# Performance work log

Hardware: AMD Instinct MI355X
Metric: run time of the kernel (lower is better)

Reference implementation:

```python
import jax, jax.numpy as jnp
import numpy as np

N_EMBD = 512
NUM_HEADS = 8
HEAD_SIZE = 64


def setup_inputs() -> dict:
    key = jax.random.key(0)
    ks = jax.random.split(key, 6)
    B, T, C, H, D = 64, 256, N_EMBD, NUM_HEADS, HEAD_SIZE
    s = 0.02
    return {
        "x": jax.random.normal(ks[0], (B, T, C), dtype=jnp.float32),
        "wq": jax.random.normal(ks[1], (H, C, D), dtype=jnp.float32) * s,
        "wk": jax.random.normal(ks[2], (H, C, D), dtype=jnp.float32) * s,
        "wv": jax.random.normal(ks[3], (H, C, D), dtype=jnp.float32) * s,
        "bq": jnp.zeros((H, D), dtype=jnp.float32),
        "bk": jnp.zeros((H, D), dtype=jnp.float32),
        "bv": jnp.zeros((H, D), dtype=jnp.float32),
        "wo": jax.random.normal(ks[4], (H * D, C), dtype=jnp.float32) * s,
        "bo": jnp.zeros((C,), dtype=jnp.float32),
    }


def reference(x, wq, wk, wv, bq, bk, bv, wo, bo):
    B, T, C = x.shape
    H, _, D = wq.shape
    # per-head QKV projections (vectorized over heads)
    q = jnp.einsum('btc,hcd->bhtd', x, wq) + bq[None, :, None, :]
    k = jnp.einsum('btc,hcd->bhtd', x, wk) + bk[None, :, None, :]
    v = jnp.einsum('btc,hcd->bhtd', x, wv) + bv[None, :, None, :]
    scale = 1.0 / jnp.sqrt(jnp.asarray(D, dtype=x.dtype))
    scores = jnp.einsum('bhtd,bhsd->bhts', q, k) * scale  # [B,H,T,T]
    causal = jnp.tril(jnp.ones((T, T), dtype=bool))
    scores = jnp.where(causal[None, None], scores, -jnp.inf)
    weights = jax.nn.softmax(scores, axis=-1)  # dropout omitted (eval mode)
    out = jnp.einsum('bhts,bhsd->bhtd', weights, v)  # [B,H,T,D]
    combined = out.transpose(0, 2, 1, 3).reshape(B, T, H * D)
    return combined @ wo + bo
```

## Files before the change

### kernel.cpp

```cpp
#include <hip/hip_runtime.h>

typedef unsigned int   u32;
typedef unsigned short u16;
typedef __attribute__((ext_vector_type(8))) short short8;
typedef __attribute__((ext_vector_type(4))) float f32x4;


__device__ __forceinline__ u16 f2bf(float f) {
    u32 u = __float_as_uint(f);
    u += 0x7fffu + ((u >> 16) & 1u);
    return (u16)(u >> 16);
}

__device__ __forceinline__ void gload_lds16(const u16* g, u16* l) {
    __builtin_amdgcn_global_load_lds(
        (const __attribute__((address_space(1))) u32*)(const void*)g,
        (__attribute__((address_space(3))) u32*)(void*)l, 16, 0, 0);
}

__global__ void cast_x_kernel(const float* __restrict__ x, u16* __restrict__ xb) {
    int i = blockIdx.x * 256 + threadIdx.x;
    float4 v = ((const float4*)x)[i];
    ushort4 o;
    o.x = f2bf(v.x); o.y = f2bf(v.y); o.z = f2bf(v.z); o.w = f2bf(v.w);
    ((ushort4*)xb)[i] = o;
}

__global__ void pack_wqkv_kernel(const float* __restrict__ wq, const float* __restrict__ wk,
                                 const float* __restrict__ wv, u16* __restrict__ wt) {
    int i = blockIdx.x * 256 + threadIdx.x;
    int n = i >> 9, c = i & 511;
    int proj = n >> 9, hd = n & 511;
    int h = hd >> 6, d = hd & 63;
    const float* w = (proj == 0) ? wq : (proj == 1) ? wk : wv;
    wt[(size_t)n * 512 + c] = f2bf(w[h * 32768 + c * 64 + d]);
}

__global__ void pack_wo_kernel(const float* __restrict__ wo, u16* __restrict__ wt) {
    int i = blockIdx.x * 256 + threadIdx.x;
    int n = i >> 9, k = i & 511;
    wt[(size_t)n * 512 + k] = f2bf(wo[(size_t)k * 512 + n]);
}

template<int EPI, int NT>
__global__ __launch_bounds__(256)
void gemm128_kernel(const u16* __restrict__ A, const u16* __restrict__ Bt,
                    float* __restrict__ outf, const float* __restrict__ bo,
                    u16* __restrict__ Qb, u16* __restrict__ Kb, u16* __restrict__ Vb,
                    const float* __restrict__ bq, const float* __restrict__ bk,
                    const float* __restrict__ bv) {
    __shared__ __align__(16) u16 As[128 * 32];
    __shared__ __align__(16) u16 Bs[128 * 32];
    const int tid = threadIdx.x;
    const int bid = blockIdx.x;
    const int xcd = bid & 7;
    const int k8  = bid >> 3;
    const int m0 = (xcd * 16 + k8 / NT) * 128;
    const int n0 = (k8 % NT) * 128;
    const int lrow = tid >> 2;
    const int seg  = tid & 3;
    const int xsw  = (lrow >> 1) & 3;
    const u16* Ag = A  + (size_t)(m0 + lrow) * 512 + (seg ^ xsw) * 8;
    const u16* Bg = Bt + (size_t)(n0 + lrow) * 512 + (seg ^ xsw) * 8;
    u16* Asl = As + lrow * 32 + seg * 8;
    u16* Bsl = Bs + lrow * 32 + seg * 8;

    const int w = tid >> 6, lane = tid & 63;
    const int wrow = (w >> 1) * 64, wcol = (w & 1) * 64;
    const int lm = lane & 15, quad = lane >> 4;
    const int kx = (quad ^ ((lm >> 1) & 3)) * 8;

    f32x4 acc[4][4] = {};

    for (int kt = 0; kt < 16; ++kt) {
        __syncthreads();
        gload_lds16(Ag + kt * 32,             Asl);
        gload_lds16(Ag + 64 * 512 + kt * 32,  Asl + 64 * 32);
        gload_lds16(Bg + kt * 32,             Bsl);
        gload_lds16(Bg + 64 * 512 + kt * 32,  Bsl + 64 * 32);
        __syncthreads();
        short8 af[4], bf[4];
        #pragma unroll
        for (int mi = 0; mi < 4; ++mi)
            af[mi] = *(const short8*)(As + (wrow + mi * 16 + lm) * 32 + kx);
        #pragma unroll
        for (int ni = 0; ni < 4; ++ni)
            bf[ni] = *(const short8*)(Bs + (wcol + ni * 16 + lm) * 32 + kx);
        #pragma unroll
        for (int mi = 0; mi < 4; ++mi)
            #pragma unroll
            for (int ni = 0; ni < 4; ++ni)
                acc[mi][ni] = __builtin_amdgcn_mfma_f32_16x16x32_bf16(af[mi], bf[ni], acc[mi][ni], 0, 0, 0);
    }

    if (EPI == 1) {
        #pragma unroll
        for (int ni = 0; ni < 4; ++ni) {
            int ncol = n0 + wcol + ni * 16 + lm;
            float bias = bo[ncol];
            #pragma unroll
            for (int mi = 0; mi < 4; ++mi) {
                int mbase = m0 + wrow + mi * 16 + quad * 4;
                #pragma unroll
                for (int r = 0; r < 4; ++r)
                    outf[(size_t)(mbase + r) * 512 + ncol] = acc[mi][ni][r] + bias;
            }
        }
    } else {
        #pragma unroll
        for (int ni = 0; ni < 4; ++ni) {
            int ncol = n0 + wcol + ni * 16 + lm;
            int proj = ncol >> 9, hd = ncol & 511;
            int h = hd >> 6, d = hd & 63;
            const float* bptr = (proj == 0) ? bq : (proj == 1) ? bk : bv;
            u16* dst = (proj == 0) ? Qb : (proj == 1) ? Kb : Vb;
            float bias = bptr[hd];
            #pragma unroll
            for (int mi = 0; mi < 4; ++mi) {
                int mbase = m0 + wrow + mi * 16 + quad * 4;
                #pragma unroll
                for (int r = 0; r < 4; ++r) {
                    int mrow = mbase + r;
                    int b = mrow >> 8, t = mrow & 255;
                    size_t idx = (proj == 2)
                        ? ((size_t)((b * 8 + h) * 64 + d) * 256 + t)
                        : ((size_t)((b * 8 + h) * 256 + t) * 64 + d);
                    dst[idx] = f2bf(acc[mi][ni][r] + bias);
                }
            }
        }
    }
}

__global__ __launch_bounds__(256)
void attn_mfma_kernel(const u16* __restrict__ Qg, const u16* __restrict__ Kg,
                      const u16* __restrict__ Vtg, u16* __restrict__ attn) {
    __shared__ __align__(16) u16 lds[20480];
    const int bid = blockIdx.x;
    const int head = (bid & 7) * 64 + ((bid >> 3) >> 1);
    const int iset = (bid >> 3) & 1;
    const int b = head >> 3, h = head & 7;
    const int tid = threadIdx.x;
    const size_t hb = (size_t)head * 16384;

    {
        const uint4* Ksrc = (const uint4*)(Kg + hb);
        uint4* L4 = (uint4*)lds;
        #pragma unroll
        for (int it = 0; it < 8; ++it) {
            int g = it * 256 + tid;
            int kr = g >> 3, kc = g & 7;
            L4[kr * 8 + (kc ^ (kr & 7))] = Ksrc[g];
        }
    }
    __syncthreads();

    const int w = tid >> 6, lane = tid & 63;
    const int lm = lane & 15, quad = lane >> 4;
    const int l7 = lm & 7;

    const int kx0 = (quad ^ l7) * 8;
    const int kx1 = ((4 + quad) ^ l7) * 8;
    const u16* Kbase = lds + lm * 64;
    const u16* Vg = Vtg + hb;
    const int Pbase = 16384 + w * 1024;
    const int x0 = (lm >> 3) & 1;
    const int pw_even = Pbase + quad * 16 + l7 + x0 * 8;
    const int pw_odd  = Pbase + quad * 16 + l7 + (x0 ^ 1) * 8;
    const int pr0 = Pbase + ((lm & 3) * 4 + (quad >> 1)) * 64
                  + (2 * (lm >> 2) + ((quad & 1) ^ (lm & 1))) * 8;

    #pragma unroll 1
    for (int ii = 0; ii < 2; ++ii) {
        const int i = iset ? (ii ? 2 : 1) : (ii ? 3 : 0);
        const int t0 = i * 64 + w * 16;
        short8 qa0 = *(const short8*)(Qg + hb + (size_t)(t0 + lm) * 64 + quad * 8);
        short8 qa1 = *(const short8*)(Qg + hb + (size_t)(t0 + lm) * 64 + 32 + quad * 8);
        f32x4 O[4] = {};
        float mr[4] = {-INFINITY, -INFINITY, -INFINITY, -INFINITY};
        float lr[4] = {0.f, 0.f, 0.f, 0.f};

        #pragma unroll 1
        for (int j = 0; j <= i; ++j) {
            f32x4 S[4] = {};
            #pragma unroll
            for (int ni = 0; ni < 4; ++ni) {
                const u16* kp = Kbase + j * 4096 + ni * 1024;
                short8 kb0 = *(const short8*)(kp + kx0);
                short8 kb1 = *(const short8*)(kp + kx1);
                S[ni] = __builtin_amdgcn_mfma_f32_16x16x32_bf16(qa0, kb0, S[ni], 0, 0, 0);
                S[ni] = __builtin_amdgcn_mfma_f32_16x16x32_bf16(qa1, kb1, S[ni], 0, 0, 0);
            }
            if (j == i) {
                #pragma unroll
                for (int ni = 0; ni < 4; ++ni) {
                    int scol = ni * 16 + lm;
                    #pragma unroll
                    for (int rr = 0; rr < 4; ++rr) {
                        int tloc = w * 16 + quad * 4 + rr;
                        S[ni][rr] = (scol > tloc) ? -INFINITY : S[ni][rr] * 0.125f;
                    }
                }
            } else {
                #pragma unroll
                for (int ni = 0; ni < 4; ++ni)
                    #pragma unroll
                    for (int rr = 0; rr < 4; ++rr)
                        S[ni][rr] *= 0.125f;
            }
            float alpha[4];
            #pragma unroll
            for (int rr = 0; rr < 4; ++rr) {
                float mx = fmaxf(fmaxf(S[0][rr], S[1][rr]), fmaxf(S[2][rr], S[3][rr]));
                mx = fmaxf(mx, __shfl_xor(mx, 1));
                mx = fmaxf(mx, __shfl_xor(mx, 2));
                mx = fmaxf(mx, __shfl_xor(mx, 4));
                mx = fmaxf(mx, __shfl_xor(mx, 8));
                float mnew = fmaxf(mr[rr], mx);
                alpha[rr] = __expf(mr[rr] - mnew);
                mr[rr] = mnew;
            }
            float rs[4] = {0.f, 0.f, 0.f, 0.f};
            #pragma unroll
            for (int ni = 0; ni < 4; ++ni) {
                #pragma unroll
                for (int rr = 0; rr < 4; ++rr) {
                    float p = __expf(S[ni][rr] - mr[rr]);
                    rs[rr] += p;
                    int addr = ((rr & 1) ? pw_odd : pw_even) + (rr * 4 + ni) * 64;
                    lds[addr] = f2bf(p);
                }
            }
            #pragma unroll
            for (int rr = 0; rr < 4; ++rr) {
                float s = rs[rr];
                s += __shfl_xor(s, 1);
                s += __shfl_xor(s, 2);
                s += __shfl_xor(s, 4);
                s += __shfl_xor(s, 8);
                lr[rr] = lr[rr] * alpha[rr] + s;
                O[0][rr] *= alpha[rr]; O[1][rr] *= alpha[rr];
                O[2][rr] *= alpha[rr]; O[3][rr] *= alpha[rr];
            }
            __syncthreads();
            short8 pa0 = *(const short8*)(lds + pr0);
            short8 pa1 = *(const short8*)(lds + pr0 + 128);
            #pragma unroll
            for (int nd = 0; nd < 4; ++nd) {
                const u16* vp = Vg + (size_t)(nd * 16 + lm) * 256 + j * 64;
                short8 vb0 = *(const short8*)(vp + quad * 8);
                short8 vb1 = *(const short8*)(vp + 32 + quad * 8);
                O[nd] = __builtin_amdgcn_mfma_f32_16x16x32_bf16(pa0, vb0, O[nd], 0, 0, 0);
                O[nd] = __builtin_amdgcn_mfma_f32_16x16x32_bf16(pa1, vb1, O[nd], 0, 0, 0);
            }
        }
        #pragma unroll
        for (int rr = 0; rr < 4; ++rr) {
            float inv = 1.0f / lr[rr];
            int t = t0 + quad * 4 + rr;
            u16* op = attn + (size_t)(b * 256 + t) * 512 + h * 64 + lm;
            op[0]  = f2bf(O[0][rr] * inv);
            op[16] = f2bf(O[1][rr] * inv);
            op[32] = f2bf(O[2][rr] * inv);
            op[48] = f2bf(O[3][rr] * inv);
        }
    }
}

extern "C" void kernel_launch(void* const* d_in, const int* in_sizes, int n_in,
                              void* d_out, int out_size, void* d_ws, size_t ws_size,
                              hipStream_t stream) {
    const float* x  = (const float*)d_in[0];
    const float* wq = (const float*)d_in[1];
    const float* wk = (const float*)d_in[2];
    const float* wv = (const float*)d_in[3];
    const float* bq = (const float*)d_in[4];
    const float* bk = (const float*)d_in[5];
    const float* bv = (const float*)d_in[6];
    const float* wo = (const float*)d_in[7];
    const float* bo = (const float*)d_in[8];
    float* out = (float*)d_out;

    char* ws = (char*)d_ws;
    const size_t SZ = 16777216;
    u16* xb    = (u16*)(ws);
    u16* Qb    = (u16*)(ws + SZ);
    u16* Kb    = (u16*)(ws + 2 * SZ);
    u16* Vt    = (u16*)(ws + 3 * SZ);
    u16* attn  = (u16*)(ws + 4 * SZ);
    u16* wqkvT = (u16*)(ws + 5 * SZ);
    u16* woT   = (u16*)(ws + 5 * SZ + 1572864);

    cast_x_kernel<<<8192, 256, 0, stream>>>(x, xb);
    pack_wqkv_kernel<<<3072, 256, 0, stream>>>(wq, wk, wv, wqkvT);
    pack_wo_kernel<<<1024, 256, 0, stream>>>(wo, woT);

    gemm128_kernel<0, 12><<<1536, 256, 0, stream>>>(
        xb, wqkvT, nullptr, nullptr, Qb, Kb, Vt, bq, bk, bv);

    attn_mfma_kernel<<<1024, 256, 0, stream>>>(Qb, Kb, Vt, attn);

    gemm128_kernel<1, 4><<<512, 256, 0, stream>>>(
        attn, woT, out, bo, nullptr, nullptr, nullptr, nullptr, nullptr, nullptr);
}
```

Before: 211.3 us.

## Double-buffer LDS tiles in GEMM to overlap global loads with MFMA

```diff
diff --git a/kernel.cpp b/kernel.cpp
--- a/kernel.cpp
+++ b/kernel.cpp
@@ -49,8 +49,8 @@
                     u16* __restrict__ Qb, u16* __restrict__ Kb, u16* __restrict__ Vb,
                     const float* __restrict__ bq, const float* __restrict__ bk,
                     const float* __restrict__ bv) {
-    __shared__ __align__(16) u16 As[128 * 32];
-    __shared__ __align__(16) u16 Bs[128 * 32];
+    __shared__ __align__(16) u16 As[2][128 * 32];
+    __shared__ __align__(16) u16 Bs[2][128 * 32];
     const int tid = threadIdx.x;
     const int bid = blockIdx.x;
     const int xcd = bid & 7;
@@ -62,8 +62,7 @@
     const int xsw  = (lrow >> 1) & 3;
     const u16* Ag = A  + (size_t)(m0 + lrow) * 512 + (seg ^ xsw) * 8;
     const u16* Bg = Bt + (size_t)(n0 + lrow) * 512 + (seg ^ xsw) * 8;
-    u16* Asl = As + lrow * 32 + seg * 8;
-    u16* Bsl = Bs + lrow * 32 + seg * 8;
+    const int lofs = lrow * 32 + seg * 8;
 
     const int w = tid >> 6, lane = tid & 63;
     const int wrow = (w >> 1) * 64, wcol = (w & 1) * 64;
@@ -72,20 +71,33 @@
 
     f32x4 acc[4][4] = {};
 
+    gload_lds16(Ag,            As[0] + lofs);
+    gload_lds16(Ag + 64 * 512, As[0] + lofs + 64 * 32);
+    gload_lds16(Bg,            Bs[0] + lofs);
+    gload_lds16(Bg + 64 * 512, Bs[0] + lofs + 64 * 32);
+
+    #pragma unroll 2
     for (int kt = 0; kt < 16; ++kt) {
         __syncthreads();
-        gload_lds16(Ag + kt * 32,             Asl);
-        gload_lds16(Ag + 64 * 512 + kt * 32,  Asl + 64 * 32);
-        gload_lds16(Bg + kt * 32,             Bsl);
-        gload_lds16(Bg + 64 * 512 + kt * 32,  Bsl + 64 * 32);
-        __syncthreads();
+        if (kt < 15) {
+            const u16* Agp = Ag + (kt + 1) * 32;
+            const u16* Bgp = Bg + (kt + 1) * 32;
+            u16* Asp = As[(kt + 1) & 1] + lofs;
+            u16* Bsp = Bs[(kt + 1) & 1] + lofs;
+            gload_lds16(Agp,            Asp);
+            gload_lds16(Agp + 64 * 512, Asp + 64 * 32);
+            gload_lds16(Bgp,            Bsp);
+            gload_lds16(Bgp + 64 * 512, Bsp + 64 * 32);
+        }
+        const u16* Ac = As[kt & 1];
+        const u16* Bc = Bs[kt & 1];
         short8 af[4], bf[4];
         #pragma unroll
         for (int mi = 0; mi < 4; ++mi)
-            af[mi] = *(const short8*)(As + (wrow + mi * 16 + lm) * 32 + kx);
+            af[mi] = *(const short8*)(Ac + (wrow + mi * 16 + lm) * 32 + kx);
         #pragma unroll
         for (int ni = 0; ni < 4; ++ni)
-            bf[ni] = *(const short8*)(Bs + (wcol + ni * 16 + lm) * 32 + kx);
+            bf[ni] = *(const short8*)(Bc + (wcol + ni * 16 + lm) * 32 + kx);
         #pragma unroll
         for (int mi = 0; mi < 4; ++mi)
             #pragma unroll
```

Measured after the change: 211.7 us. About the same (+0.2%).

## Drop LDS staging in GEMMs and attention, load operands directly from global

Applied to the files above, without the earlier changes.

```diff
diff --git a/kernel.cpp b/kernel.cpp
--- a/kernel.cpp
+++ b/kernel.cpp
@@ -10,12 +10,6 @@
     u32 u = __float_as_uint(f);
     u += 0x7fffu + ((u >> 16) & 1u);
     return (u16)(u >> 16);
-}
-
-__device__ __forceinline__ void gload_lds16(const u16* g, u16* l) {
-    __builtin_amdgcn_global_load_lds(
-        (const __attribute__((address_space(1))) u32*)(const void*)g,
-        (__attribute__((address_space(3))) u32*)(void*)l, 16, 0, 0);
 }
 
 __global__ void cast_x_kernel(const float* __restrict__ x, u16* __restrict__ xb) {
@@ -42,92 +36,111 @@
     wt[(size_t)n * 512 + k] = f2bf(wo[(size_t)k * 512 + n]);
 }
 
-template<int EPI, int NT>
+__device__ __forceinline__ void ldf(const u16* Ap0, const u16* Bp0, int kt,
+                                    short8* af, short8* bf) {
+    #pragma unroll
+    for (int mi = 0; mi < 4; ++mi) af[mi] = *(const short8*)(Ap0 + mi * 8192 + kt * 32);
+    #pragma unroll
+    for (int ni = 0; ni < 4; ++ni) bf[ni] = *(const short8*)(Bp0 + ni * 8192 + kt * 32);
+}
+__device__ __forceinline__ void mm16(const short8* af, const short8* bf, f32x4 acc[4][4]) {
+    #pragma unroll
+    for (int mi = 0; mi < 4; ++mi)
+        #pragma unroll
+        for (int ni = 0; ni < 4; ++ni)
+            acc[mi][ni] = __builtin_amdgcn_mfma_f32_16x16x32_bf16(af[mi], bf[ni], acc[mi][ni], 0, 0, 0);
+}
+
 __global__ __launch_bounds__(256)
-void gemm128_kernel(const u16* __restrict__ A, const u16* __restrict__ Bt,
-                    float* __restrict__ outf, const float* __restrict__ bo,
-                    u16* __restrict__ Qb, u16* __restrict__ Kb, u16* __restrict__ Vb,
-                    const float* __restrict__ bq, const float* __restrict__ bk,
-                    const float* __restrict__ bv) {
-    __shared__ __align__(16) u16 As[128 * 32];
-    __shared__ __align__(16) u16 Bs[128 * 32];
+void gemm_qkv(const u16* __restrict__ A, const u16* __restrict__ Bt,
+              u16* __restrict__ Qb, u16* __restrict__ Kb, u16* __restrict__ Vb,
+              const float* __restrict__ bq, const float* __restrict__ bk,
+              const float* __restrict__ bv) {
     const int tid = threadIdx.x;
     const int bid = blockIdx.x;
     const int xcd = bid & 7;
     const int k8  = bid >> 3;
-    const int m0 = (xcd * 16 + k8 / NT) * 128;
-    const int n0 = (k8 % NT) * 128;
-    const int lrow = tid >> 2;
-    const int seg  = tid & 3;
-    const int xsw  = (lrow >> 1) & 3;
-    const u16* Ag = A  + (size_t)(m0 + lrow) * 512 + (seg ^ xsw) * 8;
-    const u16* Bg = Bt + (size_t)(n0 + lrow) * 512 + (seg ^ xsw) * 8;
-    u16* Asl = As + lrow * 32 + seg * 8;
-    u16* Bsl = Bs + lrow * 32 + seg * 8;
-
+    const int m0 = (xcd * 16 + k8 / 12) * 128;
+    const int n0 = (k8 % 12) * 128;
     const int w = tid >> 6, lane = tid & 63;
     const int wrow = (w >> 1) * 64, wcol = (w & 1) * 64;
     const int lm = lane & 15, quad = lane >> 4;
-    const int kx = (quad ^ ((lm >> 1) & 3)) * 8;
+
+    const u16* Ap0 = A  + (size_t)(m0 + wrow + lm) * 512 + quad * 8;
+    const u16* Bp0 = Bt + (size_t)(n0 + wcol + lm) * 512 + quad * 8;
 
     f32x4 acc[4][4] = {};
-
-    for (int kt = 0; kt < 16; ++kt) {
-        __syncthreads();
-        gload_lds16(Ag + kt * 32,             Asl);
-        gload_lds16(Ag + 64 * 512 + kt * 32,  Asl + 64 * 32);
-        gload_lds16(Bg + kt * 32,             Bsl);
-        gload_lds16(Bg + 64 * 512 + kt * 32,  Bsl + 64 * 32);
-        __syncthreads();
-        short8 af[4], bf[4];
+    short8 aA[4], bA[4], aB[4], bB[4];
+    ldf(Ap0, Bp0, 0, aA, bA);
+    #pragma unroll
+    for (int kt = 0; kt < 16; kt += 2) {
+        if (kt + 1 < 16) ldf(Ap0, Bp0, kt + 1, aB, bB);
+        mm16(aA, bA, acc);
+        if (kt + 2 < 16) ldf(Ap0, Bp0, kt + 2, aA, bA);
+        mm16(aB, bB, acc);
+    }
+
+    #pragma unroll
+    for (int ni = 0; ni < 4; ++ni) {
+        int ncol = n0 + wcol + ni * 16 + lm;
+        int proj = ncol >> 9, hd = ncol & 511;
+        int h = hd >> 6, d = hd & 63;
+        const float* bptr = (proj == 0) ? bq : (proj == 1) ? bk : bv;
+        u16* dst = (proj == 0) ? Qb : (proj == 1) ? Kb : Vb;
+        float bias = bptr[hd];
         #pragma unroll
-        for (int mi = 0; mi < 4; ++mi)
-            af[mi] = *(const short8*)(As + (wrow + mi * 16 + lm) * 32 + kx);
+        for (int mi = 0; mi < 4; ++mi) {
+            int mbase = m0 + wrow + mi * 16 + quad * 4;
+            #pragma unroll
+            for (int r = 0; r < 4; ++r) {
+                int mrow = mbase + r;
+                int b = mrow >> 8, t = mrow & 255;
+                size_t idx = (proj == 2)
+                    ? ((size_t)((b * 8 + h) * 64 + d) * 256 + t)
+                    : ((size_t)((b * 8 + h) * 256 + t) * 64 + d);
+                dst[idx] = f2bf(acc[mi][ni][r] + bias);
+            }
+        }
+    }
+}
+
+__global__ __launch_bounds__(256)
+void gemm_out(const u16* __restrict__ A, const u16* __restrict__ Bt,
+              float* __restrict__ outf, const float* __restrict__ bo) {
+    const int tid = threadIdx.x;
+    const int bid = blockIdx.x;
+    const int xcd = bid & 7;
+    const int k8  = bid >> 3;
+    const int m0 = (xcd * 16 + k8 / 4) * 128;
+    const int n0 = (k8 % 4) * 128;
+    const int w = tid >> 6, lane = tid & 63;
+    const int wrow = (w >> 1) * 64, wcol = (w & 1) * 64;
+    const int lm = lane & 15, quad = lane >> 4;
+
+    const u16* Ap0 = A  + (size_t)(m0 + wrow + lm) * 512 + quad * 8;
+    const u16* Bp0 = Bt + (size_t)(n0 + wcol + lm) * 512 + quad * 8;
+
+    f32x4 acc[4][4] = {};
+    short8 aA[4], bA[4], aB[4], bB[4];
+    ldf(Ap0, Bp0, 0, aA, bA);
+    #pragma unroll
+    for (int kt = 0; kt < 16; kt += 2) {
+        if (kt + 1 < 16) ldf(Ap0, Bp0, kt + 1, aB, bB);
+        mm16(aA, bA, acc);
+        if (kt + 2 < 16) ldf(Ap0, Bp0, kt + 2, aA, bA);
+        mm16(aB, bB, acc);
+    }
+
+    #pragma unroll
+    for (int ni = 0; ni < 4; ++ni) {
+        int ncol = n0 + wcol + ni * 16 + lm;
+        float bias = bo[ncol];
         #pragma unroll
-        for (int ni = 0; ni < 4; ++ni)
-            bf[ni] = *(const short8*)(Bs + (wcol + ni * 16 + lm) * 32 + kx);
-        #pragma unroll
-        for (int mi = 0; mi < 4; ++mi)
-            #pragma unroll
-            for (int ni = 0; ni < 4; ++ni)
-                acc[mi][ni] = __builtin_amdgcn_mfma_f32_16x16x32_bf16(af[mi], bf[ni], acc[mi][ni], 0, 0, 0);
-    }
-
-    if (EPI == 1) {
-        #pragma unroll
-        for (int ni = 0; ni < 4; ++ni) {
-            int ncol = n0 + wcol + ni * 16 + lm;
-            float bias = bo[ncol];
-            #pragma unroll
-            for (int mi = 0; mi < 4; ++mi) {
-                int mbase = m0 + wrow + mi * 16 + quad * 4;
-                #pragma unroll
-                for (int r = 0; r < 4; ++r)
-                    outf[(size_t)(mbase + r) * 512 + ncol] = acc[mi][ni][r] + bias;
-            }
-        }
-    } else {
-        #pragma unroll
-        for (int ni = 0; ni < 4; ++ni) {
-            int ncol = n0 + wcol + ni * 16 + lm;
-            int proj = ncol >> 9, hd = ncol & 511;
-            int h = hd >> 6, d = hd & 63;
-            const float* bptr = (proj == 0) ? bq : (proj == 1) ? bk : bv;
-            u16* dst = (proj == 0) ? Qb : (proj == 1) ? Kb : Vb;
-            float bias = bptr[hd];
-            #pragma unroll
-            for (int mi = 0; mi < 4; ++mi) {
-                int mbase = m0 + wrow + mi * 16 + quad * 4;
-                #pragma unroll
-                for (int r = 0; r < 4; ++r) {
-                    int mrow = mbase + r;
-                    int b = mrow >> 8, t = mrow & 255;
-                    size_t idx = (proj == 2)
-                        ? ((size_t)((b * 8 + h) * 64 + d) * 256 + t)
-                        : ((size_t)((b * 8 + h) * 256 + t) * 64 + d);
-                    dst[idx] = f2bf(acc[mi][ni][r] + bias);
-                }
-            }
+        for (int mi = 0; mi < 4; ++mi) {
+            int mbase = m0 + wrow + mi * 16 + quad * 4;
+            #pragma unroll
+            for (int r = 0; r < 4; ++r)
+                outf[(size_t)(mbase + r) * 512 + ncol] = acc[mi][ni][r] + bias;
         }
     }
 }
@@ -135,7 +148,7 @@
 __global__ __launch_bounds__(256)
 void attn_mfma_kernel(const u16* __restrict__ Qg, const u16* __restrict__ Kg,
                       const u16* __restrict__ Vtg, u16* __restrict__ attn) {
-    __shared__ __align__(16) u16 lds[20480];
+    __shared__ __align__(16) u16 lds[4096];
     const int bid = blockIdx.x;
     const int head = (bid & 7) * 64 + ((bid >> 3) >> 1);
     const int iset = (bid >> 3) & 1;
@@ -143,27 +156,13 @@
     const int tid = threadIdx.x;
     const size_t hb = (size_t)head * 16384;
 
-    {
-        const uint4* Ksrc = (const uint4*)(Kg + hb);
-        uint4* L4 = (uint4*)lds;
-        #pragma unroll
-        for (int it = 0; it < 8; ++it) {
-            int g = it * 256 + tid;
-            int kr = g >> 3, kc = g & 7;
-            L4[kr * 8 + (kc ^ (kr & 7))] = Ksrc[g];
-        }
-    }
-    __syncthreads();
-
     const int w = tid >> 6, lane = tid & 63;
     const int lm = lane & 15, quad = lane >> 4;
     const int l7 = lm & 7;
 
-    const int kx0 = (quad ^ l7) * 8;
-    const int kx1 = ((4 + quad) ^ l7) * 8;
-    const u16* Kbase = lds + lm * 64;
-    const u16* Vg = Vtg + hb;
-    const int Pbase = 16384 + w * 1024;
+    const u16* Kgh = Kg + hb;
+    const u16* Vg  = Vtg + hb;
+    const int Pbase = w * 1024;
     const int x0 = (lm >> 3) & 1;
     const int pw_even = Pbase + quad * 16 + l7 + x0 * 8;
     const int pw_odd  = Pbase + quad * 16 + l7 + (x0 ^ 1) * 8;
@@ -185,11 +184,18 @@
             f32x4 S[4] = {};
             #pragma unroll
             for (int ni = 0; ni < 4; ++ni) {
-                const u16* kp = Kbase + j * 4096 + ni * 1024;
-                short8 kb0 = *(const short8*)(kp + kx0);
-                short8 kb1 = *(const short8*)(kp + kx1);
+                const u16* kp = Kgh + (size_t)(j * 64 + ni * 16 + lm) * 64;
+                short8 kb0 = *(const short8*)(kp + quad * 8);
+                short8 kb1 = *(const short8*)(kp + 32 + quad * 8);
                 S[ni] = __builtin_amdgcn_mfma_f32_16x16x32_bf16(qa0, kb0, S[ni], 0, 0, 0);
                 S[ni] = __builtin_amdgcn_mfma_f32_16x16x32_bf16(qa1, kb1, S[ni], 0, 0, 0);
+            }
+            short8 vb[4][2];
+            #pragma unroll
+            for (int nd = 0; nd < 4; ++nd) {
+                const u16* vp = Vg + (size_t)(nd * 16 + lm) * 256 + j * 64;
+                vb[nd][0] = *(const short8*)(vp + quad * 8);
+                vb[nd][1] = *(const short8*)(vp + 32 + quad * 8);
             }
             if (j == i) {
                 #pragma unroll
@@ -247,11 +253,8 @@
             short8 pa1 = *(const short8*)(lds + pr0 + 128);
             #pragma unroll
             for (int nd = 0; nd < 4; ++nd) {
-                const u16* vp = Vg + (size_t)(nd * 16 + lm) * 256 + j * 64;
-                short8 vb0 = *(const short8*)(vp + quad * 8);
-                short8 vb1 = *(const short8*)(vp + 32 + quad * 8);
-                O[nd] = __builtin_amdgcn_mfma_f32_16x16x32_bf16(pa0, vb0, O[nd], 0, 0, 0);
-                O[nd] = __builtin_amdgcn_mfma_f32_16x16x32_bf16(pa1, vb1, O[nd], 0, 0, 0);
+                O[nd] = __builtin_amdgcn_mfma_f32_16x16x32_bf16(pa0, vb[nd][0], O[nd], 0, 0, 0);
+                O[nd] = __builtin_amdgcn_mfma_f32_16x16x32_bf16(pa1, vb[nd][1], O[nd], 0, 0, 0);
             }
         }
         #pragma unroll
@@ -295,11 +298,9 @@
     pack_wqkv_kernel<<<3072, 256, 0, stream>>>(wq, wk, wv, wqkvT);
     pack_wo_kernel<<<1024, 256, 0, stream>>>(wo, woT);
 
-    gemm128_kernel<0, 12><<<1536, 256, 0, stream>>>(
-        xb, wqkvT, nullptr, nullptr, Qb, Kb, Vt, bq, bk, bv);
+    gemm_qkv<<<1536, 256, 0, stream>>>(xb, wqkvT, Qb, Kb, Vt, bq, bk, bv);
 
     attn_mfma_kernel<<<1024, 256, 0, stream>>>(Qb, Kb, Vt, attn);
 
-    gemm128_kernel<1, 4><<<512, 256, 0, stream>>>(
-        attn, woT, out, bo, nullptr, nullptr, nullptr, nullptr, nullptr, nullptr);
-}
+    gemm_out<<<512, 256, 0, stream>>>(attn, woT, out, bo);
+}
```

Measured after the change: 301.3 us. 1.43x slower.
